# Performance work log

Hardware: AMD Instinct MI355X
Metric: run time of the kernel (lower is better)

The kernel has to match this reference:

```python
import jax, jax.numpy as jnp
import numpy as np
import random

EPS = 1e-16  # matches EKM eps default
B, M, N, R = 8, 8192, 512, 256


def setup_inputs() -> dict:
    key = jax.random.key(0)
    kx, = jax.random.split(key, 1)
    x = jax.random.normal(kx, (B, M, N), dtype=jnp.float32)
    # EKM init: random.seed(42); inds = random.sample(range(M), R)
    random.seed(42)
    inds = jnp.asarray(random.sample(range(M), R), dtype=jnp.int32)
    # EKMInit overrides ekm.alpha with nn.Parameter(torch.tensor([0.1]))
    alpha = jnp.asarray([0.1], dtype=jnp.float32)
    return {"x": x, "alpha": alpha, "inds": inds}


def _memberships(x, v, alpha):
    x2 = jnp.sum(x * x, axis=2, keepdims=True)           # (B, M, 1)
    xv = jnp.einsum('bmn,bnr->bmr', x, v)                # (B, M, R)
    v2 = jnp.sum(v * v, axis=1, keepdims=True)           # (B, 1, R)
    d = jax.nn.relu(x2 - 2.0 * xv + v2)
    return jax.nn.softmax(-d / alpha, axis=2)            # (B, M, R)


def reference(x, alpha, inds):
    # init: v0 = t(x[:, inds, :]) -> (B, N, R); u0 = memberships(x, v0)
    v0 = jnp.swapaxes(x[:, inds, :], 1, 2)               # (B, N, R)
    # solver step (num_iters=1): u_new = memberships(x, v0) (== u0),
    # v_new = centers(x, u_new)
    u = _memberships(x, v0, alpha)                       # (B, M, R)
    u_n = (u + EPS) / (jnp.sum(u, axis=1, keepdims=True) + EPS)
    v = jnp.einsum('bmn,bmr->bnr', x, u_n)               # (B, N, R)
    return (u, v)
```

## Files before the change

kernel.cpp:

```cpp
#include <hip/hip_runtime.h>
#include <math.h>

#define B 8
#define M 8192
#define N 512
#define R 256
#define EPSF 1e-16f

typedef __attribute__((ext_vector_type(8))) short short8;
typedef __attribute__((ext_vector_type(16))) float f32x16;

__device__ __forceinline__ unsigned short bf16_rtn(float f) {
    unsigned int u = __float_as_uint(f);
    u += 0x7FFFu + ((u >> 16) & 1u);
    return (unsigned short)(u >> 16);
}

__device__ __forceinline__ void gll16(const unsigned short* g, unsigned short* l) {
    __builtin_amdgcn_global_load_lds(
        (const __attribute__((address_space(1))) unsigned int*)g,
        (__attribute__((address_space(3))) unsigned int*)l, 16, 0, 0);
}

__global__ __launch_bounds__(256) void ekm_kc(
    const float* __restrict__ x, const int* __restrict__ inds,
    unsigned short* __restrict__ c_hi, unsigned short* __restrict__ c_lo,
    float* __restrict__ v2g)
{
    const int t = threadIdx.x, b = blockIdx.y;
    const int r = blockIdx.x * 16 + (t >> 4);
    const int seg = (t & 15) * 32;
    const float* src = x + ((size_t)b * M + inds[r]) * N + seg;
    unsigned short* hd = c_hi + ((size_t)b * R + r) * 512 + seg;
    unsigned short* ld = c_lo + ((size_t)b * R + r) * 512 + seg;
    float vp = 0.f;
#pragma unroll
    for (int c = 0; c < 4; ++c) {
        float4 f0 = *(const float4*)(src + c * 8);
        float4 f1 = *(const float4*)(src + c * 8 + 4);
        float av[8] = {f0.x, f0.y, f0.z, f0.w, f1.x, f1.y, f1.z, f1.w};
        unsigned ph[4], pl[4];
#pragma unroll
        for (int j = 0; j < 4; ++j) {
            vp += av[2*j] * av[2*j] + av[2*j+1] * av[2*j+1];
            unsigned short h0 = bf16_rtn(av[2*j]), h1 = bf16_rtn(av[2*j+1]);
            float r0 = av[2*j]   - __uint_as_float((unsigned)h0 << 16);
            float r1 = av[2*j+1] - __uint_as_float((unsigned)h1 << 16);
            ph[j] = (unsigned)h0 | ((unsigned)h1 << 16);
            pl[j] = (unsigned)bf16_rtn(r0) | ((unsigned)bf16_rtn(r1) << 16);
        }
        *(uint4*)(hd + c * 8) = make_uint4(ph[0], ph[1], ph[2], ph[3]);
        *(uint4*)(ld + c * 8) = make_uint4(pl[0], pl[1], pl[2], pl[3]);
    }
    vp += __shfl_xor(vp, 1); vp += __shfl_xor(vp, 2);
    vp += __shfl_xor(vp, 4); vp += __shfl_xor(vp, 8);
    if ((t & 15) == 0) v2g[b * R + r] = vp;
}

__global__ __launch_bounds__(256, 3) void ekm_k1(
    const float* __restrict__ x, const float* __restrict__ alpha_p,
    const unsigned short* __restrict__ c_hi, const unsigned short* __restrict__ c_lo,
    const float* __restrict__ v2g, float* __restrict__ u_out,
    unsigned short* __restrict__ uT, unsigned short* __restrict__ xT,
    float* __restrict__ colsum)
{
    __shared__ unsigned short Ah[64 * 40], Al[64 * 40];
    __shared__ unsigned short Bh[256 * 32], Bl[256 * 32];
    __shared__ float x2s[64];
    __shared__ float redm[4][64], reds[4][64];

    const int t = threadIdx.x;
    const int b = blockIdx.y;
    const int m0 = blockIdx.x * 64;
    const int w = t >> 6, l = t & 63, col = l & 31, h5 = l >> 5;
    const int arow = t >> 2, kch = t & 3;

    const float* ax = x + ((size_t)b * M + m0 + arow) * N + kch * 8;
    const unsigned short* bhs = c_hi + ((size_t)b * R + (t >> 2)) * 512 + (t & 3) * 8;
    const unsigned short* bls = c_lo + ((size_t)b * R + (t >> 2)) * 512 + (t & 3) * 8;

    f32x16 acc[2][2];
    acc[0][0] = (f32x16)0.f; acc[0][1] = (f32x16)0.f;
    acc[1][0] = (f32x16)0.f; acc[1][1] = (f32x16)0.f;

    float x2p = 0.f;

    for (int k0 = 0; k0 < N; k0 += 32) {
        float4 a0 = *(const float4*)(ax + k0);
        float4 a1 = *(const float4*)(ax + k0 + 4);
        x2p += a0.x*a0.x + a0.y*a0.y + a0.z*a0.z + a0.w*a0.w
             + a1.x*a1.x + a1.y*a1.y + a1.z*a1.z + a1.w*a1.w;
        float av[8] = {a0.x, a0.y, a0.z, a0.w, a1.x, a1.y, a1.z, a1.w};
        unsigned ph[4], pl[4];
#pragma unroll
        for (int j = 0; j < 4; ++j) {
            unsigned short h0 = bf16_rtn(av[2*j]), h1 = bf16_rtn(av[2*j+1]);
            float r0 = av[2*j]   - __uint_as_float((unsigned)h0 << 16);
            float r1 = av[2*j+1] - __uint_as_float((unsigned)h1 << 16);
            ph[j] = (unsigned)h0 | ((unsigned)h1 << 16);
            pl[j] = (unsigned)bf16_rtn(r0) | ((unsigned)bf16_rtn(r1) << 16);
        }
        __syncthreads();
#pragma unroll
        for (int i = 0; i < 4; ++i) {
            gll16(bhs + k0 + i * (64 * 512), Bh + i * 2048 + t * 8);
            gll16(bls + k0 + i * (64 * 512), Bl + i * 2048 + t * 8);
        }
        *(uint4*)&Ah[arow * 40 + kch * 8] = make_uint4(ph[0], ph[1], ph[2], ph[3]);
        *(uint4*)&Al[arow * 40 + kch * 8] = make_uint4(pl[0], pl[1], pl[2], pl[3]);
        __syncthreads();

        {
            int kk = t >> 3, ms = (t & 7) * 8;
            unsigned q0 = (unsigned)Ah[(ms+0)*40+kk] | ((unsigned)Ah[(ms+1)*40+kk] << 16);
            unsigned q1 = (unsigned)Ah[(ms+2)*40+kk] | ((unsigned)Ah[(ms+3)*40+kk] << 16);
            unsigned q2 = (unsigned)Ah[(ms+4)*40+kk] | ((unsigned)Ah[(ms+5)*40+kk] << 16);
            unsigned q3 = (unsigned)Ah[(ms+6)*40+kk] | ((unsigned)Ah[(ms+7)*40+kk] << 16);
            *(uint4*)(xT + ((size_t)b * N + k0 + kk) * M + m0 + ms) = make_uint4(q0, q1, q2, q3);
        }

#pragma unroll
        for (int half = 0; half < 2; ++half) {
            short8 ah[2], al2[2], bh[2], bl2[2];
#pragma unroll
            for (int tm = 0; tm < 2; ++tm) {
                ah[tm]  = *(const short8*)&Ah[(tm*32 + col) * 40 + half*16 + h5*8];
                al2[tm] = *(const short8*)&Al[(tm*32 + col) * 40 + half*16 + h5*8];
            }
#pragma unroll
            for (int tr = 0; tr < 2; ++tr) {
                bh[tr]  = *(const short8*)&Bh[(w*64 + tr*32 + col) * 32 + half*16 + h5*8];
                bl2[tr] = *(const short8*)&Bl[(w*64 + tr*32 + col) * 32 + half*16 + h5*8];
            }
#pragma unroll
            for (int tm = 0; tm < 2; ++tm)
#pragma unroll
            for (int tr = 0; tr < 2; ++tr) {
                acc[tm][tr] = __builtin_amdgcn_mfma_f32_32x32x16_bf16(ah[tm],  bh[tr],  acc[tm][tr], 0, 0, 0);
                acc[tm][tr] = __builtin_amdgcn_mfma_f32_32x32x16_bf16(ah[tm],  bl2[tr], acc[tm][tr], 0, 0, 0);
                acc[tm][tr] = __builtin_amdgcn_mfma_f32_32x32x16_bf16(al2[tm], bh[tr],  acc[tm][tr], 0, 0, 0);
            }
        }
    }

    x2p += __shfl_xor(x2p, 1);
    x2p += __shfl_xor(x2p, 2);
    if (kch == 0) x2s[arow] = x2p;
    __syncthreads();

    const float ia = 1.4426950408889634f / alpha_p[0];
    float v2c[2];
#pragma unroll
    for (int tr = 0; tr < 2; ++tr)
        v2c[tr] = v2g[b * R + w * 64 + tr * 32 + col];

#pragma unroll
    for (int tm = 0; tm < 2; ++tm)
#pragma unroll
    for (int reg = 0; reg < 16; ++reg) {
        int rowl = (reg & 3) + 8 * (reg >> 2) + 4 * h5;
        float x2v = x2s[tm * 32 + rowl];
        float mn;
#pragma unroll
        for (int tr = 0; tr < 2; ++tr) {
            float d = x2v - 2.f * acc[tm][tr][reg] + v2c[tr];
            d = fmaxf(d, 0.f);
            acc[tm][tr][reg] = d;
            mn = (tr == 0) ? d : fminf(mn, d);
        }
        mn = fminf(mn, __shfl_xor(mn, 1));
        mn = fminf(mn, __shfl_xor(mn, 2));
        mn = fminf(mn, __shfl_xor(mn, 4));
        mn = fminf(mn, __shfl_xor(mn, 8));
        mn = fminf(mn, __shfl_xor(mn, 16));
        if (col == 0) redm[w][tm * 32 + rowl] = mn;
    }
    __syncthreads();

#pragma unroll
    for (int tm = 0; tm < 2; ++tm)
#pragma unroll
    for (int reg = 0; reg < 16; ++reg) {
        int m = tm * 32 + (reg & 3) + 8 * (reg >> 2) + 4 * h5;
        float mn = fminf(fminf(redm[0][m], redm[1][m]), fminf(redm[2][m], redm[3][m]));
        float s = 0.f;
#pragma unroll
        for (int tr = 0; tr < 2; ++tr) {
            float e = exp2f((mn - acc[tm][tr][reg]) * ia);
            acc[tm][tr][reg] = e;
            s += e;
        }
        s += __shfl_xor(s, 1); s += __shfl_xor(s, 2); s += __shfl_xor(s, 4);
        s += __shfl_xor(s, 8); s += __shfl_xor(s, 16);
        if (col == 0) reds[w][m] = s;
    }
    __syncthreads();

    float* ub = u_out + ((size_t)b * M + m0) * R + w * 64;
    float cs[2] = {0.f, 0.f};
#pragma unroll
    for (int tm = 0; tm < 2; ++tm)
#pragma unroll
    for (int reg = 0; reg < 16; ++reg) {
        int rowl = (reg & 3) + 8 * (reg >> 2) + 4 * h5;
        int m = tm * 32 + rowl;
        float inv = 1.f / (reds[0][m] + reds[1][m] + reds[2][m] + reds[3][m]);
#pragma unroll
        for (int tr = 0; tr < 2; ++tr) {
            float uu = acc[tm][tr][reg] * inv;
            acc[tm][tr][reg] = uu;
            ub[(size_t)m * R + tr * 32 + col] = uu;
            cs[tr] += uu;
        }
    }
    unsigned short* uTb = uT + ((size_t)b * R + w * 64) * M + m0;
#pragma unroll
    for (int tm = 0; tm < 2; ++tm)
#pragma unroll
    for (int tr = 0; tr < 2; ++tr)
#pragma unroll
    for (int rq = 0; rq < 4; ++rq) {
        uint2 p;
        p.x = (unsigned)bf16_rtn(acc[tm][tr][rq*4+0]) | ((unsigned)bf16_rtn(acc[tm][tr][rq*4+1]) << 16);
        p.y = (unsigned)bf16_rtn(acc[tm][tr][rq*4+2]) | ((unsigned)bf16_rtn(acc[tm][tr][rq*4+3]) << 16);
        *(uint2*)(uTb + (size_t)(tr*32 + col) * M + tm*32 + 8*rq + 4*h5) = p;
    }
    cs[0] += __shfl_xor(cs[0], 32);
    cs[1] += __shfl_xor(cs[1], 32);
    if (h5 == 0) {
        atomicAdd(&colsum[b * R + w * 64 + col], cs[0]);
        atomicAdd(&colsum[b * R + w * 64 + 32 + col], cs[1]);
    }
}

__global__ __launch_bounds__(256, 4) void ekm_k2(
    const unsigned short* __restrict__ xT, const unsigned short* __restrict__ uT,
    float* __restrict__ part)
{
    __shared__ unsigned short XA[128 * 32], UB[128 * 32];
    const int t = threadIdx.x;
    const int nt = blockIdx.x >> 1, rt = blockIdx.x & 1;
    const int slab = blockIdx.y, b = blockIdx.z;
    const int n0 = nt * 128, r0 = rt * 128;
    const int w = t >> 6, l = t & 63, col = l & 31, h5 = l >> 5;
    const int wn = w >> 1, wr = w & 1;

    const unsigned short* xs = xT + ((size_t)b * N + n0 + (t >> 2)) * M + slab * 1024 + (t & 3) * 8;
    const unsigned short* us = uT + ((size_t)b * R + r0 + (t >> 2)) * M + slab * 1024 + (t & 3) * 8;

    f32x16 acc[2][2];
    acc[0][0] = (f32x16)0.f; acc[0][1] = (f32x16)0.f;
    acc[1][0] = (f32x16)0.f; acc[1][1] = (f32x16)0.f;

    for (int k0 = 0; k0 < 1024; k0 += 32) {
        __syncthreads();
#pragma unroll
        for (int i = 0; i < 2; ++i) {
            gll16(xs + k0 + (size_t)i * 64 * M, XA + i * 2048 + t * 8);
            gll16(us + k0 + (size_t)i * 64 * M, UB + i * 2048 + t * 8);
        }
        __syncthreads();
#pragma unroll
        for (int half = 0; half < 2; ++half) {
            short8 af[2], bf2[2];
#pragma unroll
            for (int tm = 0; tm < 2; ++tm)
                af[tm] = *(const short8*)&XA[(wn*64 + tm*32 + col) * 32 + half*16 + h5*8];
#pragma unroll
            for (int tr = 0; tr < 2; ++tr)
                bf2[tr] = *(const short8*)&UB[(wr*64 + tr*32 + col) * 32 + half*16 + h5*8];
#pragma unroll
            for (int tm = 0; tm < 2; ++tm)
#pragma unroll
            for (int tr = 0; tr < 2; ++tr)
                acc[tm][tr] = __builtin_amdgcn_mfma_f32_32x32x16_bf16(af[tm], bf2[tr], acc[tm][tr], 0, 0, 0);
        }
    }

    float* pb = part + (size_t)slab * ((size_t)B * N * R) + (size_t)b * N * R;
#pragma unroll
    for (int tm = 0; tm < 2; ++tm)
#pragma unroll
    for (int reg = 0; reg < 16; ++reg) {
        int n = n0 + wn*64 + tm*32 + (reg & 3) + 8*(reg >> 2) + 4*h5;
#pragma unroll
        for (int tr = 0; tr < 2; ++tr)
            pb[(size_t)n * R + r0 + wr*64 + tr*32 + col] = acc[tm][tr][reg];
    }
}

__global__ __launch_bounds__(256) void ekm_red(
    const float* __restrict__ part, const float* __restrict__ colsum,
    float* __restrict__ v_out)
{
    size_t o = ((size_t)blockIdx.x * 256 + threadIdx.x) * 4;
    float sx = 0.f, sy = 0.f, sz = 0.f, sw = 0.f;
#pragma unroll
    for (int sl = 0; sl < 8; ++sl) {
        float4 p = *(const float4*)(part + (size_t)sl * B * N * R + o);
        sx += p.x; sy += p.y; sz += p.z; sw += p.w;
    }
    int b = (int)(o >> 17);
    int r = (int)(o & (R - 1));
    float4 cs = *(const float4*)(colsum + b * R + r);
    float4 vo;
    vo.x = sx / (cs.x + EPSF);
    vo.y = sy / (cs.y + EPSF);
    vo.z = sz / (cs.z + EPSF);
    vo.w = sw / (cs.w + EPSF);
    *(float4*)(v_out + o) = vo;
}

extern "C" void kernel_launch(void* const* d_in, const int* in_sizes, int n_in,
                              void* d_out, int out_size, void* d_ws, size_t ws_size,
                              hipStream_t stream) {
    const float* x     = (const float*)d_in[0];
    const float* alpha = (const float*)d_in[1];
    const int*   inds  = (const int*)d_in[2];

    float* u_out = (float*)d_out;
    float* v_out = u_out + (size_t)B * M * R;

    char* ws = (char*)d_ws;
    const size_t CH = (size_t)B * R * 512 * 2;
    unsigned short* c_hi   = (unsigned short*)ws;
    unsigned short* c_lo   = (unsigned short*)(ws + CH);
    float*          v2g    = (float*)(ws + 2 * CH);
    float*          colsum = (float*)(ws + 2 * CH + (size_t)B * R * 4);
    char* p = ws + 2 * CH + 2 * (size_t)B * R * 4;
    unsigned short* xT = (unsigned short*)p;          p += (size_t)B * N * M * 2;
    unsigned short* uT = (unsigned short*)p;          p += (size_t)B * R * M * 2;
    float*          part = (float*)p;

    hipMemsetAsync(colsum, 0, (size_t)B * R * sizeof(float), stream);

    ekm_kc<<<dim3(16, B), 256, 0, stream>>>(x, inds, c_hi, c_lo, v2g);
    ekm_k1<<<dim3(M / 64, B), 256, 0, stream>>>(x, alpha, c_hi, c_lo, v2g,
                                                u_out, uT, xT, colsum);
    ekm_k2<<<dim3(8, 8, B), 256, 0, stream>>>(xT, uT, part);
    ekm_red<<<(B * N * R / 4) / 256, 256, 0, stream>>>(part, colsum, v_out);
}
```

Measured before the change: 359.0 us.

## Swizzle LDS chunk layout in GEMM kernels and prefetch next x tile

Applies an XOR swizzle to the 16-byte chunk placement used by global_load_lds into the B tiles of k1 and both tiles of k2. The MFMA fragment reads use the matching swizzled index, which is meant to remove LDS bank conflicts on the 32-short row stride. In k1 the next x float4 pair is loaded after the barrier so its global latency overlaps the MFMA work. k2's launch bounds hint drops from 4 to 2 blocks per CU, which gives the compiler more registers but may lower occupancy.

```diff
diff --git a/kernel.cpp b/kernel.cpp
--- a/kernel.cpp
+++ b/kernel.cpp
@@ -74,20 +74,22 @@
     const int m0 = blockIdx.x * 64;
     const int w = t >> 6, l = t & 63, col = l & 31, h5 = l >> 5;
     const int arow = t >> 2, kch = t & 3;
+    const int cswz = (t & 3) ^ ((t >> 3) & 3);
+    const int pswz = (col >> 1) & 3;
 
     const float* ax = x + ((size_t)b * M + m0 + arow) * N + kch * 8;
-    const unsigned short* bhs = c_hi + ((size_t)b * R + (t >> 2)) * 512 + (t & 3) * 8;
-    const unsigned short* bls = c_lo + ((size_t)b * R + (t >> 2)) * 512 + (t & 3) * 8;
+    const unsigned short* bhs = c_hi + ((size_t)b * R + (t >> 2)) * 512 + cswz * 8;
+    const unsigned short* bls = c_lo + ((size_t)b * R + (t >> 2)) * 512 + cswz * 8;
 
     f32x16 acc[2][2];
     acc[0][0] = (f32x16)0.f; acc[0][1] = (f32x16)0.f;
     acc[1][0] = (f32x16)0.f; acc[1][1] = (f32x16)0.f;
 
     float x2p = 0.f;
+    float4 a0 = *(const float4*)(ax);
+    float4 a1 = *(const float4*)(ax + 4);
 
     for (int k0 = 0; k0 < N; k0 += 32) {
-        float4 a0 = *(const float4*)(ax + k0);
-        float4 a1 = *(const float4*)(ax + k0 + 4);
         x2p += a0.x*a0.x + a0.y*a0.y + a0.z*a0.z + a0.w*a0.w
              + a1.x*a1.x + a1.y*a1.y + a1.z*a1.z + a1.w*a1.w;
         float av[8] = {a0.x, a0.y, a0.z, a0.w, a1.x, a1.y, a1.z, a1.w};
@@ -109,6 +111,11 @@
         *(uint4*)&Ah[arow * 40 + kch * 8] = make_uint4(ph[0], ph[1], ph[2], ph[3]);
         *(uint4*)&Al[arow * 40 + kch * 8] = make_uint4(pl[0], pl[1], pl[2], pl[3]);
         __syncthreads();
+
+        if (k0 + 32 < N) {
+            a0 = *(const float4*)(ax + k0 + 32);
+            a1 = *(const float4*)(ax + k0 + 36);
+        }
 
         {
             int kk = t >> 3, ms = (t & 7) * 8;
@@ -121,6 +128,7 @@
 
 #pragma unroll
         for (int half = 0; half < 2; ++half) {
+            const int pc = (half * 2 + h5) ^ pswz;
             short8 ah[2], al2[2], bh[2], bl2[2];
 #pragma unroll
             for (int tm = 0; tm < 2; ++tm) {
@@ -129,8 +137,8 @@
             }
 #pragma unroll
             for (int tr = 0; tr < 2; ++tr) {
-                bh[tr]  = *(const short8*)&Bh[(w*64 + tr*32 + col) * 32 + half*16 + h5*8];
-                bl2[tr] = *(const short8*)&Bl[(w*64 + tr*32 + col) * 32 + half*16 + h5*8];
+                bh[tr]  = *(const short8*)&Bh[(w*64 + tr*32 + col) * 32 + pc*8];
+                bl2[tr] = *(const short8*)&Bl[(w*64 + tr*32 + col) * 32 + pc*8];
             }
 #pragma unroll
             for (int tm = 0; tm < 2; ++tm)
@@ -233,7 +241,7 @@
     }
 }
 
-__global__ __launch_bounds__(256, 4) void ekm_k2(
+__global__ __launch_bounds__(256, 2) void ekm_k2(
     const unsigned short* __restrict__ xT, const unsigned short* __restrict__ uT,
     float* __restrict__ part)
 {
@@ -244,9 +252,11 @@
     const int n0 = nt * 128, r0 = rt * 128;
     const int w = t >> 6, l = t & 63, col = l & 31, h5 = l >> 5;
     const int wn = w >> 1, wr = w & 1;
-
-    const unsigned short* xs = xT + ((size_t)b * N + n0 + (t >> 2)) * M + slab * 1024 + (t & 3) * 8;
-    const unsigned short* us = uT + ((size_t)b * R + r0 + (t >> 2)) * M + slab * 1024 + (t & 3) * 8;
+    const int cswz = (t & 3) ^ ((t >> 3) & 3);
+    const int pswz = (col >> 1) & 3;
+
+    const unsigned short* xs = xT + ((size_t)b * N + n0 + (t >> 2)) * M + slab * 1024 + cswz * 8;
+    const unsigned short* us = uT + ((size_t)b * R + r0 + (t >> 2)) * M + slab * 1024 + cswz * 8;
 
     f32x16 acc[2][2];
     acc[0][0] = (f32x16)0.f; acc[0][1] = (f32x16)0.f;
@@ -262,13 +272,14 @@
         __syncthreads();
 #pragma unroll
         for (int half = 0; half < 2; ++half) {
+            const int pc = (half * 2 + h5) ^ pswz;
             short8 af[2], bf2[2];
 #pragma unroll
             for (int tm = 0; tm < 2; ++tm)
-                af[tm] = *(const short8*)&XA[(wn*64 + tm*32 + col) * 32 + half*16 + h5*8];
+                af[tm] = *(const short8*)&XA[(wn*64 + tm*32 + col) * 32 + pc*8];
 #pragma unroll
             for (int tr = 0; tr < 2; ++tr)
-                bf2[tr] = *(const short8*)&UB[(wr*64 + tr*32 + col) * 32 + half*16 + h5*8];
+                bf2[tr] = *(const short8*)&UB[(wr*64 + tr*32 + col) * 32 + pc*8];
 #pragma unroll
             for (int tm = 0; tm < 2; ++tm)
 #pragma unroll
```

After: 347.5 us. 3.2% less time.
